# Optimization experiments

Hardware: AMD Instinct MI355X
Metric: run time of the kernel (lower is better)

The kernel has to match this reference:

```python
import jax, jax.numpy as jnp
import numpy as np

TAU = 0.01


def setup_inputs() -> dict:
    key = jax.random.key(0)
    k1, k2 = jax.random.split(key)
    N, C = 8192, 256  # N = H*W pixels, C = feature channels
    x_feature = jax.random.normal(k1, (N, C), dtype=jnp.float32)
    y_feature = jax.random.normal(k2, (N, C), dtype=jnp.float32)
    return {"x_feature": x_feature, "y_feature": y_feature}


def reference(x_feature, y_feature):
    # Per-channel L2 normalization (dim=0 in the torch source: norm over pixels)
    x = x_feature / jnp.linalg.norm(x_feature, axis=0, keepdims=True)  # [N, C]
    y = y_feature / jnp.linalg.norm(y_feature, axis=0, keepdims=True)  # [N, C]

    # Dense pixel-pixel cosine correlation matrix
    corr = jnp.einsum('ic,jc->ij', x, y)  # [N, N]

    # Temperature-scaled stable softmax over axis=0 (columns), as in the
    # module's custom softmax (max/sum over dim=0)
    attn = jax.nn.softmax(corr / TAU, axis=0)  # [N, N]

    # Weighted retrieval; only the diagonal of (attn @ y) is kept.
    # diag(attn @ y)[k] = sum_j attn[k, j] * y[j, k] for k < C
    C = y.shape[1]
    warped_color = jnp.einsum('kj,jk->k', attn[:C, :], y[:, :C])  # [C]

    # Confidence map: row-max of the correlation matrix
    confidence_map = jnp.max(corr, axis=1)  # [N]

    return warped_color, confidence_map
```

## Files before the change

kernel.cpp:

```cpp
#include <hip/hip_runtime.h>
#include <hip/hip_bf16.h>

#define NN 8192
#define CC 256
#define ESCALE 144.26950408889634f

typedef __attribute__((ext_vector_type(8))) short short8;
typedef __attribute__((ext_vector_type(4))) float f32x4;

typedef __attribute__((address_space(3))) unsigned int lds_u32;
typedef __attribute__((address_space(1))) const unsigned int glb_u32;

__device__ __forceinline__ void gload16(const ushort* g, ushort* l) {
  __builtin_amdgcn_global_load_lds((glb_u32*)(const void*)g, (lds_u32*)(void*)l, 16, 0, 0);
}

__global__ void colsumsq_kernel(const float* __restrict__ x, const float* __restrict__ y,
                                float* __restrict__ part) {
  const int b = blockIdx.x, t = threadIdx.x;
  const float* src = (b < 256) ? x : y;
  const int bb = b & 255;
  float s = 0.f;
#pragma unroll 4
  for (int r = 0; r < 32; ++r) {
    float v = src[(size_t)(bb * 32 + r) * CC + t];
    s = fmaf(v, v, s);
  }
  part[b * CC + t] = s;
}

__global__ void finnorm_kernel(const float* __restrict__ part, float* __restrict__ inv_n) {
  const int g = blockIdx.x * 4 + (threadIdx.x >> 6);
  const int lane = threadIdx.x & 63;
  const int c = g & 255, T = g >> 8;
  float s = 0.f;
#pragma unroll
  for (int r = 0; r < 4; ++r)
    s += part[(size_t)((T << 8) + lane * 4 + r) * CC + c];
#pragma unroll
  for (int d = 1; d < 64; d <<= 1) s += __shfl_xor(s, d);
  if (lane == 0) inv_n[g] = 1.0f / sqrtf(s);
}

__global__ void normconv_kernel(const float* __restrict__ x, const float* __restrict__ y,
                                const float* __restrict__ inv_n,
                                ushort* __restrict__ xnb, ushort* __restrict__ ynb) {
  int b = blockIdx.x;
  const float* src; ushort* dst; const float* inv;
  if (b < 2048) { src = x; dst = xnb; inv = inv_n; }
  else          { src = y; dst = ynb; inv = inv_n + 256; b -= 2048; }
  const int idx = (b * 256 + threadIdx.x) * 4;
  const float4 v = *(const float4*)(src + idx);
  const int c = idx & (CC - 1);
  __hip_bfloat16 h0 = __float2bfloat16(v.x * inv[c + 0]);
  __hip_bfloat16 h1 = __float2bfloat16(v.y * inv[c + 1]);
  __hip_bfloat16 h2 = __float2bfloat16(v.z * inv[c + 2]);
  __hip_bfloat16 h3 = __float2bfloat16(v.w * inv[c + 3]);
  ushort4 o;
  o.x = *(ushort*)&h0; o.y = *(ushort*)&h1; o.z = *(ushort*)&h2; o.w = *(ushort*)&h3;
  *(ushort4*)(dst + idx) = o;
}

__global__ __launch_bounds__(256, 4)
void gemm_corr_kernel(const ushort* __restrict__ Xn, const ushort* __restrict__ Yn,
                      float* __restrict__ corr_top,
                      float* __restrict__ rowmax_part,
                      float* __restrict__ colsum_part)
{
  const int cb = blockIdx.x, rb = blockIdx.y;
  const int tid = threadIdx.x;
  const int lane = tid & 63, wid = tid >> 6;
  const int wr = wid >> 1, wc = wid & 1;
  const int q = lane >> 4;
  const int lr = lane & 15;

  __shared__ __align__(16) ushort As[128 * 64];
  __shared__ __align__(16) ushort Bs[128 * 64];
  __shared__ float redbuf[2][128];

  f32x4 acc[4][4];
#pragma unroll
  for (int m = 0; m < 4; ++m)
#pragma unroll
    for (int n = 0; n < 4; ++n) acc[m][n] = (f32x4){0.f, 0.f, 0.f, 0.f};

  const int srow0 = tid >> 3;
  const int sp = (tid & 7) ^ (srow0 & 7);
  const size_t gAb = (size_t)(rb * 128 + srow0) * CC + sp * 8;
  const size_t gBb = (size_t)(cb * 128 + srow0) * CC + sp * 8;

  auto stage = [&](int kt) {
    const int ko = kt * 64;
#pragma unroll
    for (int r = 0; r < 4; ++r) {
      gload16(Xn + gAb + r * 32 * CC + ko, &As[r * 2048 + wid * 512]);
      gload16(Yn + gBb + r * 32 * CC + ko, &Bs[r * 2048 + wid * 512]);
    }
  };

  for (int kt = 0; kt < 4; ++kt) {
    stage(kt);
    __syncthreads();
#pragma unroll
    for (int s = 0; s < 2; ++s) {
      const int sA = ((s * 4 + q) ^ (lr & 7)) * 8;
      short8 af[4], bf[4];
#pragma unroll
      for (int m = 0; m < 4; ++m)
        af[m] = *(const short8*)(&As[(wr * 64 + m * 16 + lr) * 64 + sA]);
#pragma unroll
      for (int n = 0; n < 4; ++n)
        bf[n] = *(const short8*)(&Bs[(wc * 64 + n * 16 + lr) * 64 + sA]);
#pragma unroll
      for (int m = 0; m < 4; ++m)
#pragma unroll
        for (int n = 0; n < 4; ++n)
          acc[m][n] = __builtin_amdgcn_mfma_f32_16x16x32_bf16(af[m], bf[n], acc[m][n], 0, 0, 0);
    }
    __syncthreads();
  }

  if (rb < 2) {
    const int colg = cb * 128 + wc * 64 + lr;
#pragma unroll
    for (int m = 0; m < 4; ++m) {
      const int rowg = rb * 128 + wr * 64 + m * 16 + q * 4;
#pragma unroll
      for (int n = 0; n < 4; ++n)
#pragma unroll
        for (int r = 0; r < 4; ++r)
          corr_top[(size_t)(rowg + r) * NN + colg + n * 16] = acc[m][n][r];
    }
  }

#pragma unroll
  for (int m = 0; m < 4; ++m)
#pragma unroll
    for (int r = 0; r < 4; ++r) {
      float t = fmaxf(fmaxf(acc[m][0][r], acc[m][1][r]), fmaxf(acc[m][2][r], acc[m][3][r]));
      t = fmaxf(t, __shfl_xor(t, 1));
      t = fmaxf(t, __shfl_xor(t, 2));
      t = fmaxf(t, __shfl_xor(t, 4));
      t = fmaxf(t, __shfl_xor(t, 8));
      if (lr == 0) redbuf[wc][wr * 64 + m * 16 + q * 4 + r] = t;
    }
  __syncthreads();
  if (tid < 128)
    rowmax_part[(size_t)cb * NN + rb * 128 + tid] = fmaxf(redbuf[0][tid], redbuf[1][tid]);
  __syncthreads();

#pragma unroll
  for (int n = 0; n < 4; ++n) {
    float s = 0.f;
#pragma unroll
    for (int m = 0; m < 4; ++m)
#pragma unroll
      for (int r = 0; r < 4; ++r)
        s += __builtin_amdgcn_exp2f(acc[m][n][r] * ESCALE);
    s += __shfl_xor(s, 16);
    s += __shfl_xor(s, 32);
    if (lane < 16) redbuf[wr][wc * 64 + n * 16 + lr] = s;
  }
  __syncthreads();
  if (tid < 128)
    colsum_part[(size_t)rb * NN + cb * 128 + tid] = redbuf[0][tid] + redbuf[1][tid];
}

__global__ void reduce_both_kernel(const float* __restrict__ rowmax_part,
                                   const float* __restrict__ colsum_part,
                                   float* __restrict__ out, float* __restrict__ inv_s) {
  const int g = blockIdx.x * 256 + threadIdx.x;
  if (g < 8192) {
    float m = -3.4e38f;
#pragma unroll
    for (int b = 0; b < 64; ++b) m = fmaxf(m, rowmax_part[(size_t)b * NN + g]);
    out[256 + g] = m;
  } else {
    const int j = g - 8192;
    float s = 0.f;
#pragma unroll
    for (int b = 0; b < 64; ++b) s += colsum_part[(size_t)b * NN + j];
    inv_s[j] = 1.0f / s;
  }
}

__global__ void warped_kernel(const float* __restrict__ corr_top, const float* __restrict__ inv_s,
                              const ushort* __restrict__ ynb, float* __restrict__ wpart) {
  const int b = blockIdx.x;
  const int kb = b & 31, jb = b >> 5;
  const int k0 = kb * 8;
  const int t = threadIdx.x;
  const int kk = t & 7, js = t >> 3;
  const int jbase = jb * 2048 + js;
  float p = 0.f;
#pragma unroll 4
  for (int i = 0; i < 64; ++i) {
    const int j = jbase + 32 * i;
    float c = corr_top[(size_t)(k0 + kk) * NN + j];
    float yv = __uint_as_float((unsigned)ynb[(size_t)j * CC + k0 + kk] << 16);
    p += __builtin_amdgcn_exp2f(c * ESCALE) * inv_s[j] * yv;
  }
  p += __shfl_xor(p, 8);
  p += __shfl_xor(p, 16);
  p += __shfl_xor(p, 32);
  __shared__ float lw[4][8];
  const int lane = t & 63, wid = t >> 6;
  if (lane < 8) lw[wid][lane] = p;
  __syncthreads();
  if (t < 8) wpart[jb * 256 + k0 + t] = lw[0][t] + lw[1][t] + lw[2][t] + lw[3][t];
}

__global__ void warpedfin_kernel(const float* __restrict__ wpart, float* __restrict__ out) {
  const int k = threadIdx.x;
  out[k] = wpart[k] + wpart[256 + k] + wpart[512 + k] + wpart[768 + k];
}

extern "C" void kernel_launch(void* const* d_in, const int* in_sizes, int n_in,
                              void* d_out, int out_size, void* d_ws, size_t ws_size,
                              hipStream_t stream) {
  const float* x = (const float*)d_in[0];
  const float* y = (const float*)d_in[1];
  float* out = (float*)d_out;
  char* ws = (char*)d_ws;

  ushort* xnb        = (ushort*)(ws);
  ushort* ynb        = (ushort*)(ws + (4u << 20));
  float*  corr_top   = (float*)(ws + (8u << 20));
  float*  rowmax_prt = (float*)(ws + (16u << 20));
  float*  colsum_prt = (float*)(ws + (18u << 20));
  float*  part       = (float*)(ws + (20u << 20));
  float*  inv_n      = (float*)(ws + (20u << 20) + 524288);
  float*  inv_s      = (float*)(ws + (20u << 20) + 524288 + 4096);

  colsumsq_kernel<<<512, 256, 0, stream>>>(x, y, part);
  finnorm_kernel<<<128, 256, 0, stream>>>(part, inv_n);
  normconv_kernel<<<4096, 256, 0, stream>>>(x, y, inv_n, xnb, ynb);
  gemm_corr_kernel<<<dim3(64, 64), 256, 0, stream>>>(xnb, ynb, corr_top, rowmax_prt, colsum_prt);
  reduce_both_kernel<<<64, 256, 0, stream>>>(rowmax_prt, colsum_prt, out, inv_s);
  warped_kernel<<<128, 256, 0, stream>>>(corr_top, inv_s, ynb, part);
  warpedfin_kernel<<<1, 256, 0, stream>>>(part, out);
}
```

Baseline: 79.27 us.

## Fold y normalization into x scaling and convert y to bf16 during sumsq pass

Uses the bilinearity of the correlation to move y's per-channel inverse norm onto x. x is scaled by inv_nx*inv_ny, y is converted to bf16 unnormalized inside the column-sum-of-squares pass, and the final warped output is rescaled by inv_ny. This drops the separate y normalization pass, halving the normconv kernel's traffic. The GEMM reuses the A tile LDS for its reduction buffer and raises its launch-bounds occupancy hint from 4 to 5. Precision changes slightly because the bf16 rounding now falls on differently scaled values, and the y bf16 writes in colsumsq are scalar 2-byte stores.

```diff
diff --git a/kernel.cpp b/kernel.cpp
--- a/kernel.cpp
+++ b/kernel.cpp
@@ -16,15 +16,21 @@
 }
 
 __global__ void colsumsq_kernel(const float* __restrict__ x, const float* __restrict__ y,
-                                float* __restrict__ part) {
+                                float* __restrict__ part, ushort* __restrict__ ynb) {
   const int b = blockIdx.x, t = threadIdx.x;
-  const float* src = (b < 256) ? x : y;
+  const bool isY = (b >= 256);
+  const float* src = isY ? y : x;
   const int bb = b & 255;
   float s = 0.f;
 #pragma unroll 4
   for (int r = 0; r < 32; ++r) {
-    float v = src[(size_t)(bb * 32 + r) * CC + t];
+    const size_t idx = (size_t)(bb * 32 + r) * CC + t;
+    float v = src[idx];
     s = fmaf(v, v, s);
+    if (isY) {
+      __hip_bfloat16 h = __float2bfloat16(v);
+      ynb[idx] = *(ushort*)&h;
+    }
   }
   part[b * CC + t] = s;
 }
@@ -42,26 +48,25 @@
   if (lane == 0) inv_n[g] = 1.0f / sqrtf(s);
 }
 
-__global__ void normconv_kernel(const float* __restrict__ x, const float* __restrict__ y,
-                                const float* __restrict__ inv_n,
-                                ushort* __restrict__ xnb, ushort* __restrict__ ynb) {
-  int b = blockIdx.x;
-  const float* src; ushort* dst; const float* inv;
-  if (b < 2048) { src = x; dst = xnb; inv = inv_n; }
-  else          { src = y; dst = ynb; inv = inv_n + 256; b -= 2048; }
-  const int idx = (b * 256 + threadIdx.x) * 4;
-  const float4 v = *(const float4*)(src + idx);
+__global__ void normconv_kernel(const float* __restrict__ x, const float* __restrict__ inv_n,
+                                ushort* __restrict__ xnb) {
+  const int idx = (blockIdx.x * 256 + threadIdx.x) * 4;
+  const float4 v = *(const float4*)(x + idx);
   const int c = idx & (CC - 1);
-  __hip_bfloat16 h0 = __float2bfloat16(v.x * inv[c + 0]);
-  __hip_bfloat16 h1 = __float2bfloat16(v.y * inv[c + 1]);
-  __hip_bfloat16 h2 = __float2bfloat16(v.z * inv[c + 2]);
-  __hip_bfloat16 h3 = __float2bfloat16(v.w * inv[c + 3]);
+  float s0 = inv_n[c + 0] * inv_n[256 + c + 0];
+  float s1 = inv_n[c + 1] * inv_n[256 + c + 1];
+  float s2 = inv_n[c + 2] * inv_n[256 + c + 2];
+  float s3 = inv_n[c + 3] * inv_n[256 + c + 3];
+  __hip_bfloat16 h0 = __float2bfloat16(v.x * s0);
+  __hip_bfloat16 h1 = __float2bfloat16(v.y * s1);
+  __hip_bfloat16 h2 = __float2bfloat16(v.z * s2);
+  __hip_bfloat16 h3 = __float2bfloat16(v.w * s3);
   ushort4 o;
   o.x = *(ushort*)&h0; o.y = *(ushort*)&h1; o.z = *(ushort*)&h2; o.w = *(ushort*)&h3;
-  *(ushort4*)(dst + idx) = o;
-}
-
-__global__ __launch_bounds__(256, 4)
+  *(ushort4*)(xnb + idx) = o;
+}
+
+__global__ __launch_bounds__(256, 5)
 void gemm_corr_kernel(const ushort* __restrict__ Xn, const ushort* __restrict__ Yn,
                       float* __restrict__ corr_top,
                       float* __restrict__ rowmax_part,
@@ -76,7 +81,7 @@
 
   __shared__ __align__(16) ushort As[128 * 64];
   __shared__ __align__(16) ushort Bs[128 * 64];
-  __shared__ float redbuf[2][128];
+  float* redbuf = (float*)As;
 
   f32x4 acc[4][4];
 #pragma unroll
@@ -142,11 +147,11 @@
       t = fmaxf(t, __shfl_xor(t, 2));
       t = fmaxf(t, __shfl_xor(t, 4));
       t = fmaxf(t, __shfl_xor(t, 8));
-      if (lr == 0) redbuf[wc][wr * 64 + m * 16 + q * 4 + r] = t;
+      if (lr == 0) redbuf[wc * 128 + wr * 64 + m * 16 + q * 4 + r] = t;
     }
   __syncthreads();
   if (tid < 128)
-    rowmax_part[(size_t)cb * NN + rb * 128 + tid] = fmaxf(redbuf[0][tid], redbuf[1][tid]);
+    rowmax_part[(size_t)cb * NN + rb * 128 + tid] = fmaxf(redbuf[tid], redbuf[128 + tid]);
   __syncthreads();
 
 #pragma unroll
@@ -159,11 +164,11 @@
         s += __builtin_amdgcn_exp2f(acc[m][n][r] * ESCALE);
     s += __shfl_xor(s, 16);
     s += __shfl_xor(s, 32);
-    if (lane < 16) redbuf[wr][wc * 64 + n * 16 + lr] = s;
+    if (lane < 16) redbuf[wr * 128 + wc * 64 + n * 16 + lr] = s;
   }
   __syncthreads();
   if (tid < 128)
-    colsum_part[(size_t)rb * NN + cb * 128 + tid] = redbuf[0][tid] + redbuf[1][tid];
+    colsum_part[(size_t)rb * NN + cb * 128 + tid] = redbuf[tid] + redbuf[128 + tid];
 }
 
 __global__ void reduce_both_kernel(const float* __restrict__ rowmax_part,
@@ -210,9 +215,10 @@
   if (t < 8) wpart[jb * 256 + k0 + t] = lw[0][t] + lw[1][t] + lw[2][t] + lw[3][t];
 }
 
-__global__ void warpedfin_kernel(const float* __restrict__ wpart, float* __restrict__ out) {
+__global__ void warpedfin_kernel(const float* __restrict__ wpart, const float* __restrict__ inv_ny,
+                                 float* __restrict__ out) {
   const int k = threadIdx.x;
-  out[k] = wpart[k] + wpart[256 + k] + wpart[512 + k] + wpart[768 + k];
+  out[k] = (wpart[k] + wpart[256 + k] + wpart[512 + k] + wpart[768 + k]) * inv_ny[k];
 }
 
 extern "C" void kernel_launch(void* const* d_in, const int* in_sizes, int n_in,
@@ -232,11 +238,11 @@
   float*  inv_n      = (float*)(ws + (20u << 20) + 524288);
   float*  inv_s      = (float*)(ws + (20u << 20) + 524288 + 4096);
 
-  colsumsq_kernel<<<512, 256, 0, stream>>>(x, y, part);
+  colsumsq_kernel<<<512, 256, 0, stream>>>(x, y, part, ynb);
   finnorm_kernel<<<128, 256, 0, stream>>>(part, inv_n);
-  normconv_kernel<<<4096, 256, 0, stream>>>(x, y, inv_n, xnb, ynb);
+  normconv_kernel<<<2048, 256, 0, stream>>>(x, inv_n, xnb);
   gemm_corr_kernel<<<dim3(64, 64), 256, 0, stream>>>(xnb, ynb, corr_top, rowmax_prt, colsum_prt);
   reduce_both_kernel<<<64, 256, 0, stream>>>(rowmax_prt, colsum_prt, out, inv_s);
   warped_kernel<<<128, 256, 0, stream>>>(corr_top, inv_s, ynb, part);
-  warpedfin_kernel<<<1, 256, 0, stream>>>(part, out);
-}
+  warpedfin_kernel<<<1, 256, 0, stream>>>(part, inv_n + 256, out);
+}
```

Result: slower. 87.41 us (+10.3%).
